# Performance work log

Measured on AMD Instinct MI355X. Metric: run time of the kernel, lower is better.

The kernel has to match this reference:

```python
import jax, jax.numpy as jnp
import numpy as np

B, S, D = 4, 2048, 1024
NUM_CODES = 16384


def setup_inputs() -> dict:
    key = jax.random.key(0)
    k1, k2 = jax.random.split(key)
    inputs = jax.random.normal(k1, (B, S, D), dtype=jnp.float32)
    codebook = jax.random.normal(k2, (NUM_CODES, D), dtype=jnp.float32)
    return {"inputs": inputs, "codebook": codebook, "kcodes": 8}


def reference(inputs, codebook, kcodes):
    # logits = -cdist(inputs, codebook, p=2); squared distance is monotonic
    # with euclidean distance, so top-k indices are identical (no sqrt needed).
    x2 = jnp.sum(inputs * inputs, axis=-1, keepdims=True)        # [B,S,1]
    c2 = jnp.sum(codebook * codebook, axis=-1)                   # [C]
    xc = jnp.einsum('bsd,cd->bsc', inputs, codebook)             # [B,S,C]
    logits = -(x2 - 2.0 * xc + c2)                               # -squared dist
    _, codebook_ids = jax.lax.top_k(logits, kcodes)              # [B,S,K]
    gathered = codebook[codebook_ids]                            # [B,S,K,D]
    outputs = gathered.sum(axis=-2) / kcodes                     # [B,S,D]
    return outputs, codebook_ids
```

## Files before the change

kernel.cpp:

```cpp
#include <hip/hip_runtime.h>
#include <hip/hip_bf16.h>
#include <float.h>

#define R_TOTAL 8192
#define D_DIM   1024
#define C_TOTAL 16384
#define KSEL    8
#define XN  ((size_t)R_TOTAL * D_DIM)
#define CBN ((size_t)C_TOTAL * D_DIM)
#define NSPLIT  8
#define SEGC    (C_TOTAL / NSPLIT)
#define NCHUNK  (SEGC / 256)
#define NKT     (NCHUNK * 16)
#define NC_RES  16

typedef __attribute__((ext_vector_type(8)))  short short8v;
typedef __attribute__((ext_vector_type(16))) float f32x16;

__device__ __forceinline__ unsigned short f2bf(float f) {
  unsigned u = __float_as_uint(f);
  u = (u + 0x7fffu + ((u >> 16) & 1u)) >> 16;
  return (unsigned short)u;
}

__device__ __forceinline__ void gload_lds16(const void* g, void* l) {
  __builtin_amdgcn_global_load_lds((const __attribute__((address_space(1))) void*)g,
                                   (__attribute__((address_space(3))) void*)l, 16, 0, 0);
}

__global__ __launch_bounds__(256)
void cvt_c2_kernel(const float* __restrict__ X, const float* __restrict__ CB,
                   unsigned short* __restrict__ Xb, unsigned short* __restrict__ CBb,
                   float* __restrict__ c2g) {
  const int row  = blockIdx.x * 4 + (threadIdx.x >> 6);
  const int lane = threadIdx.x & 63;
  const bool isCB = row >= R_TOTAL;
  const int rl = isCB ? row - R_TOTAL : row;
  const float* src = (isCB ? CB : X) + (size_t)rl * D_DIM;
  unsigned short* dst = (isCB ? CBb : Xb) + (size_t)rl * D_DIM;

  float ss = 0.f;
  #pragma unroll
  for (int i = 0; i < 4; ++i) {
    const float4 v = *(const float4*)(src + i * 256 + lane * 4);
    if (isCB) ss += v.x * v.x + v.y * v.y + v.z * v.z + v.w * v.w;
    ushort4 o;
    o.x = f2bf(v.x); o.y = f2bf(v.y); o.z = f2bf(v.z); o.w = f2bf(v.w);
    *(ushort4*)(dst + i * 256 + lane * 4) = o;
  }
  if (isCB) {
    #pragma unroll
    for (int off = 32; off >= 1; off >>= 1) ss += __shfl_xor(ss, off, 64);
    if (lane == 0) c2g[rl] = ss;
  }
}

__global__ __launch_bounds__(512, 2)
void gemm_topk_kernel(const unsigned short* __restrict__ Xb,
                      const unsigned short* __restrict__ CBb,
                      const float* __restrict__ c2g,
                      float* __restrict__ pval, int* __restrict__ pid) {
  extern __shared__ char smem[];
  float* c2s = (float*)(smem + 131072);

  const int t   = threadIdx.x;
  const int wid = t >> 6, l = t & 63;
  const int wr  = wid >> 2;
  const int wc  = wid & 3;
  const int l31 = l & 31, hi = l >> 5;

  const int xt    = blockIdx.x & 31;
  const int seg   = blockIdx.x >> 5;
  const int xbase = xt * 256;
  const int cb0   = seg * SEGC;

  *(float4*)&c2s[t * 4] = *(const float4*)(c2g + cb0 + t * 4);

  const int srow = t >> 3;
  const int sswz = (((t & 7) * 16) ^ ((srow & 7) << 4)) >> 1;
  const int fswz = (l & 7) << 4;

  f32x16 acc[4][2];
  float tv[2][KSEL]; int ti[2][KSEL];
  #pragma unroll
  for (int fm = 0; fm < 4; ++fm)
    #pragma unroll
    for (int fn = 0; fn < 2; ++fn)
      #pragma unroll
      for (int r = 0; r < 16; ++r) acc[fm][fn][r] = 0.f;
  #pragma unroll
  for (int fn = 0; fn < 2; ++fn)
    #pragma unroll
    for (int q = 0; q < KSEL; ++q) { tv[fn][q] = -FLT_MAX; ti[fn][q] = 0; }

  auto STAGE_A = [&](int g) {
    const int kbase = (g & 15) * 64;
    const int arow0 = cb0 + (g >> 4) * 256;
    char* As = smem + (g & 1) * 32768;
    #pragma unroll
    for (int i = 0; i < 4; ++i)
      gload_lds16(CBb + (size_t)(arow0 + i * 64 + srow) * D_DIM + kbase + sswz,
                  As + (i * 512 + t) * 16);
  };
  auto STAGE_X = [&](int g) {
    const int kbase = (g & 15) * 64;
    char* Xs = smem + 65536 + (g & 1) * 32768;
    #pragma unroll
    for (int i = 0; i < 4; ++i)
      gload_lds16(Xb + (size_t)(xbase + i * 64 + srow) * D_DIM + kbase + sswz,
                  Xs + (i * 512 + t) * 16);
  };

  short8v avE[4], bvE[2], avO[4], bvO[2];

#define READ_FRAGS(AV, BV, ABUF, XBUF, P)                                       \
  {                                                                             \
    const int kb_ = ((P) * 32 + hi * 16) ^ fswz;                                \
    _Pragma("unroll")                                                           \
    for (int fm_ = 0; fm_ < 4; ++fm_)                                           \
      AV[fm_] = *(const short8v*)((ABUF) +                                      \
                    (wr * 128 + fm_ * 32 + l31) * 128 + kb_);                   \
    _Pragma("unroll")                                                           \
    for (int fn_ = 0; fn_ < 2; ++fn_)                                           \
      BV[fn_] = *(const short8v*)((XBUF) +                                      \
                    (wc * 64 + fn_ * 32 + l31) * 128 + kb_);                    \
  }

#define MFMA8(AV, BV)                                                           \
  {                                                                             \
    __builtin_amdgcn_s_setprio(1);                                              \
    _Pragma("unroll")                                                           \
    for (int fm_ = 0; fm_ < 4; ++fm_)                                           \
      _Pragma("unroll")                                                         \
      for (int fn_ = 0; fn_ < 2; ++fn_)                                         \
        acc[fm_][fn_] = __builtin_amdgcn_mfma_f32_32x32x16_bf16(                \
            AV[fm_], BV[fn_], acc[fm_][fn_], 0, 0, 0);                          \
    __builtin_amdgcn_s_setprio(0);                                              \
    __builtin_amdgcn_sched_barrier(0);                                          \
  }

  STAGE_A(0); STAGE_X(0);
  asm volatile("s_waitcnt vmcnt(0) lgkmcnt(0)" ::: "memory");
  __builtin_amdgcn_s_barrier();
  __builtin_amdgcn_sched_barrier(0);
  READ_FRAGS(avE, bvE, (const char*)smem, (const char*)smem + 65536, 0);

  for (int g = 0; g < NKT; ++g) {
    const char* As  = smem + (g & 1) * 32768;
    const char* Xs  = smem + 65536 + (g & 1) * 32768;
    const char* Asn = smem + ((g + 1) & 1) * 32768;
    const char* Xsn = smem + 65536 + ((g + 1) & 1) * 32768;
    const bool more = (g + 1 < NKT);

    READ_FRAGS(avO, bvO, As, Xs, 1);
    if (more) STAGE_A(g + 1);
    __builtin_amdgcn_s_barrier();
    MFMA8(avE, bvE);

    READ_FRAGS(avE, bvE, As, Xs, 2);
    if (more) STAGE_X(g + 1);
    __builtin_amdgcn_s_barrier();
    MFMA8(avO, bvO);

    READ_FRAGS(avO, bvO, As, Xs, 3);
    __builtin_amdgcn_s_barrier();
    MFMA8(avE, bvE);

    asm volatile("s_waitcnt vmcnt(0)" ::: "memory");
    __builtin_amdgcn_s_barrier();
    __builtin_amdgcn_sched_barrier(0);
    if (more) READ_FRAGS(avE, bvE, Asn, Xsn, 0);
    MFMA8(avO, bvO);

    if ((g & 15) == 15) {
      const int ch = g >> 4;
      #pragma unroll
      for (int fm = 0; fm < 4; ++fm) {
        const int rloc = ch * 256 + wr * 128 + fm * 32 + hi * 4;
        const int idb  = cb0 + ch * 256 + wr * 128 + fm * 32 + hi * 4;
        #pragma unroll
        for (int q = 0; q < 4; ++q) {
          const float4 cq = *(const float4*)&c2s[rloc + q * 8];
          #pragma unroll
          for (int fn = 0; fn < 2; ++fn) {
            #pragma unroll
            for (int r = 0; r < 4; ++r) {
              const float c2v = (r == 0) ? cq.x : (r == 1) ? cq.y : (r == 2) ? cq.z : cq.w;
              const float s = 2.f * acc[fm][fn][q * 4 + r] - c2v;
              if (s > tv[fn][KSEL - 1]) {
                float cv = s; int ci = idb + q * 8 + r;
                #pragma unroll
                for (int q2 = 0; q2 < KSEL; ++q2) {
                  if (cv > tv[fn][q2]) {
                    const float t0 = tv[fn][q2]; tv[fn][q2] = cv; cv = t0;
                    const int   t1 = ti[fn][q2]; ti[fn][q2] = ci; ci = t1;
                  }
                }
              }
            }
          }
        }
      }
      #pragma unroll
      for (int fm = 0; fm < 4; ++fm)
        #pragma unroll
        for (int fn = 0; fn < 2; ++fn)
          #pragma unroll
          for (int r = 0; r < 16; ++r) acc[fm][fn][r] = 0.f;
    }
  }

#undef READ_FRAGS
#undef MFMA8

  asm volatile("s_waitcnt vmcnt(0) lgkmcnt(0)" ::: "memory");
  __builtin_amdgcn_s_barrier();
  float* mv = (float*)smem;
  int*   mi = (int*)(smem + 32768);
  #pragma unroll
  for (int fn = 0; fn < 2; ++fn) {
    const int xrL = wc * 64 + fn * 32 + l31;
    const int li  = wr * 2 + hi;
    #pragma unroll
    for (int q = 0; q < KSEL; ++q) {
      mv[xrL * 32 + li * 8 + q] = tv[fn][q];
      mi[xrL * 32 + li * 8 + q] = ti[fn][q];
    }
  }
  __syncthreads();
  if (t < 256) {
    float bvv[KSEL]; int bii[KSEL];
    #pragma unroll
    for (int q = 0; q < KSEL; ++q) { bvv[q] = -FLT_MAX; bii[q] = 0x7fffffff; }
    for (int c = 0; c < 32; ++c) {
      float cv = mv[t * 32 + c]; int ci = mi[t * 32 + c];
      if (cv > bvv[KSEL - 1] || (cv == bvv[KSEL - 1] && ci < bii[KSEL - 1])) {
        #pragma unroll
        for (int q = 0; q < KSEL; ++q) {
          if (cv > bvv[q] || (cv == bvv[q] && ci < bii[q])) {
            const float t0 = bvv[q]; bvv[q] = cv; cv = t0;
            const int   t1 = bii[q]; bii[q] = ci; ci = t1;
          }
        }
      }
    }
    const size_t base = ((size_t)(xbase + t) * NSPLIT + seg) * KSEL;
    #pragma unroll
    for (int q = 0; q < KSEL; ++q) { pval[base + q] = bvv[q]; pid[base + q] = bii[q]; }
  }
}

__global__ __launch_bounds__(256)
void rescore_kernel(const float* __restrict__ X, const float* __restrict__ CB,
                    const float* __restrict__ c2g,
                    const float* __restrict__ pval, const int* __restrict__ pid,
                    float* __restrict__ out, float* __restrict__ out_ids) {
  const int row = blockIdx.x;
  const int t = threadIdx.x;
  __shared__ float xs[D_DIM];
  __shared__ int   scid[NC_RES];
  __shared__ float sv[NC_RES];
  __shared__ int   topid[KSEL];

  *(float4*)&xs[t * 4] = *(const float4*)(X + (size_t)row * D_DIM + t * 4);

  const int ncand = NSPLIT * KSEL;

  if (t < 64) {
    float v   = pval[(size_t)row * ncand + t];
    int   idv = pid [(size_t)row * ncand + t];
    for (int it = 0; it < NC_RES; ++it) {
      float bv = v; int bid = idv;
      #pragma unroll
      for (int off = 32; off >= 1; off >>= 1) {
        float ov = __shfl_xor(bv, off, 64);
        int   oi = __shfl_xor(bid, off, 64);
        if (ov > bv || (ov == bv && oi < bid)) { bv = ov; bid = oi; }
      }
      if (t == 0) scid[it] = bid;
      if (idv == bid) v = -FLT_MAX;
    }
  }
  __syncthreads();

  const int w = t >> 6, ln = t & 63;
  for (int c = w; c < NC_RES; c += 4) {
    const int id = scid[c];
    const float* cr = CB + (size_t)id * D_DIM;
    float s = 0.f;
    #pragma unroll
    for (int i = 0; i < 4; ++i) {
      const float4 cv = *(const float4*)(cr + ln * 4 + i * 256);
      const float4 xv = *(const float4*)&xs[ln * 4 + i * 256];
      s += cv.x * xv.x + cv.y * xv.y + cv.z * xv.z + cv.w * xv.w;
    }
    #pragma unroll
    for (int off = 32; off >= 1; off >>= 1) s += __shfl_xor(s, off, 64);
    if (ln == 0) sv[c] = 2.f * s - c2g[id];
  }
  __syncthreads();

  if (t == 0) {
    float bv[KSEL]; int bi[KSEL];
    #pragma unroll
    for (int q = 0; q < KSEL; ++q) { bv[q] = -FLT_MAX; bi[q] = 0x7fffffff; }
    for (int c = 0; c < NC_RES; ++c) {
      float cv = sv[c]; int ci = scid[c];
      #pragma unroll
      for (int q = 0; q < KSEL; ++q) {
        if (cv > bv[q] || (cv == bv[q] && ci < bi[q])) {
          const float t0 = bv[q]; bv[q] = cv; cv = t0;
          const int   t1 = bi[q]; bi[q] = ci; ci = t1;
        }
      }
    }
    #pragma unroll
    for (int q = 0; q < KSEL; ++q) {
      topid[q] = bi[q];
      out_ids[(size_t)row * KSEL + q] = (float)bi[q];
    }
  }
  __syncthreads();

  float4 a = {0.f, 0.f, 0.f, 0.f};
  #pragma unroll
  for (int q = 0; q < KSEL; ++q) {
    const float4 cv = *(const float4*)(CB + (size_t)topid[q] * D_DIM + t * 4);
    a.x += cv.x; a.y += cv.y; a.z += cv.z; a.w += cv.w;
  }
  a.x *= 0.125f; a.y *= 0.125f; a.z *= 0.125f; a.w *= 0.125f;
  *(float4*)(out + (size_t)row * D_DIM + t * 4) = a;
}

extern "C" void kernel_launch(void* const* d_in, const int* in_sizes, int n_in,
                              void* d_out, int out_size, void* d_ws, size_t ws_size,
                              hipStream_t stream) {
  const float* X  = (const float*)d_in[0];
  const float* CB = (const float*)d_in[1];

  float* out     = (float*)d_out;
  float* out_ids = out + XN;

  const size_t XbB  = XN * 2;
  const size_t CBbB = CBN * 2;
  const size_t c2B  = C_TOTAL * 4;
  const size_t pvB  = (size_t)R_TOTAL * NSPLIT * KSEL * 4;

  char* p = (char*)d_ws;
  unsigned short* Xb;
  unsigned short* CBb;
  if (ws_size >= XbB + CBbB + c2B + 2 * pvB) {
    Xb  = (unsigned short*)p; p += XbB;
    CBb = (unsigned short*)p; p += CBbB;
  } else {
    CBb = (unsigned short*)d_out;
    Xb  = (unsigned short*)p; p += XbB;
  }
  float* c2   = (float*)p; p += c2B;
  float* pval = (float*)p; p += pvB;
  int*   pid  = (int*)p;

  hipLaunchKernelGGL(cvt_c2_kernel, dim3((R_TOTAL + C_TOTAL) / 4), dim3(256), 0, stream,
                     X, CB, Xb, CBb, c2);
  hipLaunchKernelGGL(gemm_topk_kernel, dim3(32 * NSPLIT), dim3(512), 136 * 1024, stream,
                     Xb, CBb, c2, pval, pid);
  hipLaunchKernelGGL(rescore_kernel, dim3(R_TOTAL), dim3(256), 0, stream,
                     X, CB, c2, pval, pid, out, out_ids);
}
```

Baseline: 542.9 us.

## Shrink GEMM-topk tiles to 128x128 with more blocks and single-buffered LDS

Replaces the 256x256 tile, 512-thread, double-buffered GEMM+topk kernel (one block per CU, 136KB LDS) with a 128x128 tile, 256-thread, single-buffered kernel. It uses 16 codebook segments and 36KB LDS, so three blocks can share a CU. The aim is to hide latency through occupancy and more blocks instead of a hand-scheduled software pipeline. In exchange, each tile reuses less data, there is no load/compute overlap inside a block, and the rescore stage must merge twice as many partial candidates (128 per row).

New measurement: 624.1 us. 15.0% more time.

```diff
diff --git a/kernel.cpp b/kernel.cpp
--- a/kernel.cpp
+++ b/kernel.cpp
@@ -8,9 +8,9 @@
 #define KSEL    8
 #define XN  ((size_t)R_TOTAL * D_DIM)
 #define CBN ((size_t)C_TOTAL * D_DIM)
-#define NSPLIT  8
-#define SEGC    (C_TOTAL / NSPLIT)
-#define NCHUNK  (SEGC / 256)
+#define NSEG    16
+#define SEGC    (C_TOTAL / NSEG)
+#define NCHUNK  (SEGC / 128)
 #define NKT     (NCHUNK * 16)
 #define NC_RES  16
 
@@ -55,23 +55,23 @@
   }
 }
 
-__global__ __launch_bounds__(512, 2)
+__global__ __launch_bounds__(256, 3)
 void gemm_topk_kernel(const unsigned short* __restrict__ Xb,
                       const unsigned short* __restrict__ CBb,
                       const float* __restrict__ c2g,
                       float* __restrict__ pval, int* __restrict__ pid) {
   extern __shared__ char smem[];
-  float* c2s = (float*)(smem + 131072);
+  float* c2s = (float*)(smem + 32768);
 
   const int t   = threadIdx.x;
   const int wid = t >> 6, l = t & 63;
-  const int wr  = wid >> 2;
-  const int wc  = wid & 3;
+  const int wr  = wid >> 1;
+  const int wc  = wid & 1;
   const int l31 = l & 31, hi = l >> 5;
 
-  const int xt    = blockIdx.x & 31;
-  const int seg   = blockIdx.x >> 5;
-  const int xbase = xt * 256;
+  const int xt    = blockIdx.x & 63;
+  const int seg   = blockIdx.x >> 6;
+  const int xbase = xt * 128;
   const int cb0   = seg * SEGC;
 
   *(float4*)&c2s[t * 4] = *(const float4*)(c2g + cb0 + t * 4);
@@ -80,10 +80,10 @@
   const int sswz = (((t & 7) * 16) ^ ((srow & 7) << 4)) >> 1;
   const int fswz = (l & 7) << 4;
 
-  f32x16 acc[4][2];
+  f32x16 acc[2][2];
   float tv[2][KSEL]; int ti[2][KSEL];
   #pragma unroll
-  for (int fm = 0; fm < 4; ++fm)
+  for (int fm = 0; fm < 2; ++fm)
     #pragma unroll
     for (int fn = 0; fn < 2; ++fn)
       #pragma unroll
@@ -95,89 +95,44 @@
 
   auto STAGE_A = [&](int g) {
     const int kbase = (g & 15) * 64;
-    const int arow0 = cb0 + (g >> 4) * 256;
-    char* As = smem + (g & 1) * 32768;
+    const int arow0 = cb0 + (g >> 4) * 128;
     #pragma unroll
     for (int i = 0; i < 4; ++i)
-      gload_lds16(CBb + (size_t)(arow0 + i * 64 + srow) * D_DIM + kbase + sswz,
-                  As + (i * 512 + t) * 16);
+      gload_lds16(CBb + (size_t)(arow0 + i * 32 + srow) * D_DIM + kbase + sswz,
+                  smem + (i * 256 + t) * 16);
   };
   auto STAGE_X = [&](int g) {
     const int kbase = (g & 15) * 64;
-    char* Xs = smem + 65536 + (g & 1) * 32768;
     #pragma unroll
     for (int i = 0; i < 4; ++i)
-      gload_lds16(Xb + (size_t)(xbase + i * 64 + srow) * D_DIM + kbase + sswz,
-                  Xs + (i * 512 + t) * 16);
+      gload_lds16(Xb + (size_t)(xbase + i * 32 + srow) * D_DIM + kbase + sswz,
+                  smem + 16384 + (i * 256 + t) * 16);
   };
 
-  short8v avE[4], bvE[2], avO[4], bvO[2];
-
-#define READ_FRAGS(AV, BV, ABUF, XBUF, P)                                       \
-  {                                                                             \
-    const int kb_ = ((P) * 32 + hi * 16) ^ fswz;                                \
-    _Pragma("unroll")                                                           \
-    for (int fm_ = 0; fm_ < 4; ++fm_)                                           \
-      AV[fm_] = *(const short8v*)((ABUF) +                                      \
-                    (wr * 128 + fm_ * 32 + l31) * 128 + kb_);                   \
-    _Pragma("unroll")                                                           \
-    for (int fn_ = 0; fn_ < 2; ++fn_)                                           \
-      BV[fn_] = *(const short8v*)((XBUF) +                                      \
-                    (wc * 64 + fn_ * 32 + l31) * 128 + kb_);                    \
-  }
-
-#define MFMA8(AV, BV)                                                           \
-  {                                                                             \
-    __builtin_amdgcn_s_setprio(1);                                              \
-    _Pragma("unroll")                                                           \
-    for (int fm_ = 0; fm_ < 4; ++fm_)                                           \
-      _Pragma("unroll")                                                         \
-      for (int fn_ = 0; fn_ < 2; ++fn_)                                         \
-        acc[fm_][fn_] = __builtin_amdgcn_mfma_f32_32x32x16_bf16(                \
-            AV[fm_], BV[fn_], acc[fm_][fn_], 0, 0, 0);                          \
-    __builtin_amdgcn_s_setprio(0);                                              \
-    __builtin_amdgcn_sched_barrier(0);                                          \
-  }
-
-  STAGE_A(0); STAGE_X(0);
-  asm volatile("s_waitcnt vmcnt(0) lgkmcnt(0)" ::: "memory");
-  __builtin_amdgcn_s_barrier();
-  __builtin_amdgcn_sched_barrier(0);
-  READ_FRAGS(avE, bvE, (const char*)smem, (const char*)smem + 65536, 0);
-
   for (int g = 0; g < NKT; ++g) {
-    const char* As  = smem + (g & 1) * 32768;
-    const char* Xs  = smem + 65536 + (g & 1) * 32768;
-    const char* Asn = smem + ((g + 1) & 1) * 32768;
-    const char* Xsn = smem + 65536 + ((g + 1) & 1) * 32768;
-    const bool more = (g + 1 < NKT);
-
-    READ_FRAGS(avO, bvO, As, Xs, 1);
-    if (more) STAGE_A(g + 1);
-    __builtin_amdgcn_s_barrier();
-    MFMA8(avE, bvE);
-
-    READ_FRAGS(avE, bvE, As, Xs, 2);
-    if (more) STAGE_X(g + 1);
-    __builtin_amdgcn_s_barrier();
-    MFMA8(avO, bvO);
-
-    READ_FRAGS(avO, bvO, As, Xs, 3);
-    __builtin_amdgcn_s_barrier();
-    MFMA8(avE, bvE);
-
-    asm volatile("s_waitcnt vmcnt(0)" ::: "memory");
-    __builtin_amdgcn_s_barrier();
-    __builtin_amdgcn_sched_barrier(0);
-    if (more) READ_FRAGS(avE, bvE, Asn, Xsn, 0);
-    MFMA8(avO, bvO);
+    __syncthreads();
+    STAGE_A(g); STAGE_X(g);
+    __syncthreads();
+
+    #pragma unroll
+    for (int ks = 0; ks < 4; ++ks) {
+      const int kb = (ks * 32 + hi * 16) ^ fswz;
+      short8v a0 = *(const short8v*)(smem + (wr * 64 +      l31) * 128 + kb);
+      short8v a1 = *(const short8v*)(smem + (wr * 64 + 32 + l31) * 128 + kb);
+      short8v b0 = *(const short8v*)(smem + 16384 + (wc * 64 +      l31) * 128 + kb);
+      short8v b1 = *(const short8v*)(smem + 16384 + (wc * 64 + 32 + l31) * 128 + kb);
+      acc[0][0] = __builtin_amdgcn_mfma_f32_32x32x16_bf16(a0, b0, acc[0][0], 0, 0, 0);
+      acc[0][1] = __builtin_amdgcn_mfma_f32_32x32x16_bf16(a0, b1, acc[0][1], 0, 0, 0);
+      acc[1][0] = __builtin_amdgcn_mfma_f32_32x32x16_bf16(a1, b0, acc[1][0], 0, 0, 0);
+      acc[1][1] = __builtin_amdgcn_mfma_f32_32x32x16_bf16(a1, b1, acc[1][1], 0, 0, 0);
+    }
 
     if ((g & 15) == 15) {
       const int ch = g >> 4;
       #pragma unroll
-      for (int fm = 0; fm < 4; ++fm) {
-        const int rloc = ch * 256 + wr * 128 + fm * 32 + hi * 4;
-        const int idb  = cb0 + ch * 256 + wr * 128 + fm * 32 + hi * 4;
+      for (int fm = 0; fm < 2; ++fm) {
+        const int rloc = ch * 128 + wr * 64 + fm * 32 + hi * 4;
+        const int idb  = cb0 + rloc;
         #pragma unroll
         for (int q = 0; q < 4; ++q) {
           const float4 cq = *(const float4*)&c2s[rloc + q * 8];
@@ -202,7 +157,7 @@
         }
       }
       #pragma unroll
-      for (int fm = 0; fm < 4; ++fm)
+      for (int fm = 0; fm < 2; ++fm)
         #pragma unroll
         for (int fn = 0; fn < 2; ++fn)
           #pragma unroll
@@ -210,13 +165,9 @@
     }
   }
 
-#undef READ_FRAGS
-#undef MFMA8
-
-  asm volatile("s_waitcnt vmcnt(0) lgkmcnt(0)" ::: "memory");
-  __builtin_amdgcn_s_barrier();
+  __syncthreads();
   float* mv = (float*)smem;
-  int*   mi = (int*)(smem + 32768);
+  int*   mi = (int*)(smem + 16384);
   #pragma unroll
   for (int fn = 0; fn < 2; ++fn) {
     const int xrL = wc * 64 + fn * 32 + l31;
@@ -228,7 +179,7 @@
     }
   }
   __syncthreads();
-  if (t < 256) {
+  if (t < 128) {
     float bvv[KSEL]; int bii[KSEL];
     #pragma unroll
     for (int q = 0; q < KSEL; ++q) { bvv[q] = -FLT_MAX; bii[q] = 0x7fffffff; }
@@ -244,7 +195,7 @@
         }
       }
     }
-    const size_t base = ((size_t)(xbase + t) * NSPLIT + seg) * KSEL;
+    const size_t base = ((size_t)(xbase + t) * NSEG + seg) * KSEL;
     #pragma unroll
     for (int q = 0; q < KSEL; ++q) { pval[base + q] = bvv[q]; pid[base + q] = bii[q]; }
   }
@@ -264,13 +215,17 @@
 
   *(float4*)&xs[t * 4] = *(const float4*)(X + (size_t)row * D_DIM + t * 4);
 
-  const int ncand = NSPLIT * KSEL;
+  const int ncand = NSEG * KSEL;
 
   if (t < 64) {
-    float v   = pval[(size_t)row * ncand + t];
-    int   idv = pid [(size_t)row * ncand + t];
+    float v0 = pval[(size_t)row * ncand + t];
+    int   i0 = pid [(size_t)row * ncand + t];
+    float v1 = pval[(size_t)row * ncand + t + 64];
+    int   i1 = pid [(size_t)row * ncand + t + 64];
     for (int it = 0; it < NC_RES; ++it) {
-      float bv = v; int bid = idv;
+      float bv; int bid;
+      if (v0 > v1 || (v0 == v1 && i0 < i1)) { bv = v0; bid = i0; }
+      else                                  { bv = v1; bid = i1; }
       #pragma unroll
       for (int off = 32; off >= 1; off >>= 1) {
         float ov = __shfl_xor(bv, off, 64);
@@ -278,7 +233,8 @@
         if (ov > bv || (ov == bv && oi < bid)) { bv = ov; bid = oi; }
       }
       if (t == 0) scid[it] = bid;
-      if (idv == bid) v = -FLT_MAX;
+      if (i0 == bid) v0 = -FLT_MAX;
+      if (i1 == bid) v1 = -FLT_MAX;
     }
   }
   __syncthreads();
@@ -344,7 +300,7 @@
   const size_t XbB  = XN * 2;
   const size_t CBbB = CBN * 2;
   const size_t c2B  = C_TOTAL * 4;
-  const size_t pvB  = (size_t)R_TOTAL * NSPLIT * KSEL * 4;
+  const size_t pvB  = (size_t)R_TOTAL * NSEG * KSEL * 4;
 
   char* p = (char*)d_ws;
   unsigned short* Xb;
@@ -362,7 +318,7 @@
 
   hipLaunchKernelGGL(cvt_c2_kernel, dim3((R_TOTAL + C_TOTAL) / 4), dim3(256), 0, stream,
                      X, CB, Xb, CBb, c2);
-  hipLaunchKernelGGL(gemm_topk_kernel, dim3(32 * NSPLIT), dim3(512), 136 * 1024, stream,
+  hipLaunchKernelGGL(gemm_topk_kernel, dim3(64 * NSEG), dim3(256), 36 * 1024, stream,
                      Xb, CBb, c2, pval, pid);
   hipLaunchKernelGGL(rescore_kernel, dim3(R_TOTAL), dim3(256), 0, stream,
                      X, CB, c2, pval, pid, out, out_ids);
```
